# Kernel tuning notes

Hardware: AMD Instinct MI355X
Metric: run time of the kernel (lower is better)

The kernel has to match this reference:

```python
import jax, jax.numpy as jnp
import numpy as np

D_EMB = 256


def setup_inputs() -> dict:
    key = jax.random.key(0)
    ks = jax.random.split(key, 7)
    B, S, d = 4, 4096, D_EMB
    scale = 1.0 / np.sqrt(d)
    return {
        "x": jax.random.normal(ks[0], (B, S, d), jnp.float32),
        "Wqkv": jax.random.normal(ks[1], (d, 3 * d), jnp.float32) * scale,
        "bqkv": jax.random.normal(ks[2], (3 * d,), jnp.float32) * 0.02,
        "Wproj": jax.random.normal(ks[3], (d, d), jnp.float32) * scale,
        "bproj": jax.random.normal(ks[4], (d,), jnp.float32) * 0.02,
        "Wfc": jax.random.normal(ks[5], (d, 1), jnp.float32) * scale,
        "bfc": jax.random.normal(ks[6], (1,), jnp.float32) * 0.02,
    }


def reference(x, Wqkv, bqkv, Wproj, bproj, Wfc, bfc):
    # qkv projection: [B,S,3d] -> split into q,k,v [B,S,d]
    qkv = x @ Wqkv + bqkv
    q, k, v = jnp.split(qkv, 3, axis=2)
    # full attention scores [B,S,S]; note: original applies NO 1/sqrt(d)
    # scaling (dead branch in source), 'traditional' softmax over last dim
    attn_scores = jnp.einsum("bqd,bkd->bqk", q, k)
    attn_weights = jax.nn.softmax(attn_scores, axis=-1)
    y = jnp.einsum("bqk,bkd->bqd", attn_weights, v)
    y = y @ Wproj + bproj
    out = y @ Wfc + bfc  # [B,S,1]
    return out
```

## Files before the change

### kernel.cpp

```cpp
#include <hip/hip_runtime.h>
#include <hip/hip_bf16.h>

#define BQ 4
#define SQ 4096
#define DQ 256
#define N3 768
#define KBLK 64
#define NITER (SQ / KBLK)
#define KHALF (NITER / 2)
#define LOG2E 1.44269504f
#define THR2 11.5415603f

typedef __attribute__((ext_vector_type(8))) _Float16 f16x8;
typedef __attribute__((ext_vector_type(4))) float f32x4;
typedef __attribute__((ext_vector_type(4))) unsigned int u32x4;

__device__ __forceinline__ short f2h(float f) {
  _Float16 h = (_Float16)f;
  union { _Float16 h; short s; } v; v.h = h;
  return v.s;
}

__device__ __forceinline__ void gload16(const void* g, void* lds) {
  __builtin_amdgcn_global_load_lds(
      (const __attribute__((address_space(1))) unsigned int*)g,
      (__attribute__((address_space(3))) unsigned int*)lds, 16, 0, 0);
}

__global__ void wcomb_kernel(const float* __restrict__ Wproj,
                             const float* __restrict__ bproj,
                             const float* __restrict__ Wfc,
                             const float* __restrict__ bfc,
                             float* __restrict__ Wc) {
  __shared__ float wf[256];
  const int t = threadIdx.x;
  wf[t] = Wfc[t];
  __syncthreads();
  float acc = 0.f;
  for (int j = 0; j < 256; ++j) acc += Wproj[(size_t)t * 256 + j] * wf[j];
  Wc[t] = acc;
  if (t == 0) {
    float c = bfc[0];
    for (int j = 0; j < 256; ++j) c += bproj[j] * wf[j];
    Wc[256] = c;
  }
}

__global__ void wconv_kernel(const float* __restrict__ Wqkv,
                             short* __restrict__ W16T) {
  __shared__ float tile[64][65];
  const int nb = blockIdx.x * 64;
  const int kb = blockIdx.y * 64;
  const int t = threadIdx.x;
  const int tr = t >> 6, tc = t & 63;
#pragma unroll
  for (int i = 0; i < 16; ++i)
    tile[tr + i * 4][tc] = Wqkv[(size_t)(kb + tr + i * 4) * N3 + nb + tc];
  __syncthreads();
#pragma unroll
  for (int i = 0; i < 16; ++i)
    W16T[(size_t)(nb + tr + i * 4) * 256 + kb + tc] = f2h(tile[tc][tr + i * 4]);
}

__global__ __launch_bounds__(1024, 4) void qkv_kernel(
    const float* __restrict__ x, const short* __restrict__ W16T,
    const float* __restrict__ bqkv, const float* __restrict__ Wc,
    short* __restrict__ Qb, short* __restrict__ Kb, float* __restrict__ u) {
  __shared__ short xs[64][264];
  __shared__ short ws[2][64][256];
  __shared__ float u_red[4][4][16];
  const int t = threadIdx.x;
  const int l = t & 63, w = t >> 6;
  const int lr = l & 15, lg = l >> 4;
  const int mq = w >> 2, nq = w & 3;
  const int Mbase = blockIdx.x * 64;

#define STAGE_W(BUF, NT)                                                      \
  {                                                                           \
    _Pragma("unroll") for (int i = 0; i < 2; ++i) {                           \
      const int n = w * 4 + i * 2 + (l >> 5);                                 \
      const int gc = (l & 31) ^ (n & 7);                                      \
      gload16(W16T + (size_t)((NT)*64 + n) * 256 + gc * 8,                    \
              &ws[BUF][w * 4 + i * 2][0]);                                    \
    }                                                                         \
  }

  STAGE_W(0, 0);

  {
    const int m = t >> 4, kc = (t & 15) * 16;
    const float* src = x + (size_t)(Mbase + m) * DQ + kc;
    short tmp[16];
#pragma unroll
    for (int i = 0; i < 16; ++i) tmp[i] = f2h(src[i]);
    *(u32x4*)&xs[m][kc] = *(u32x4*)&tmp[0];
    *(u32x4*)&xs[m][kc + 8] = *(u32x4*)&tmp[8];
  }

  float bias_qk[8], bias_u[4], wc_u[4];
#pragma unroll
  for (int i = 0; i < 8; ++i) bias_qk[i] = bqkv[i * 64 + nq * 16 + lr];
#pragma unroll
  for (int i = 0; i < 4; ++i) {
    bias_u[i] = bqkv[512 + i * 64 + nq * 16 + lr];
    wc_u[i] = Wc[i * 64 + nq * 16 + lr];
  }

  __syncthreads();

  unsigned qksto[8][2];
  float upart[4] = {0.f, 0.f, 0.f, 0.f};

#pragma unroll
  for (int nt = 0; nt < 12; ++nt) {
    const int cur = nt & 1;
    if (nt + 1 < 12) {
      STAGE_W(cur ^ 1, nt + 1);
      asm volatile("s_waitcnt vmcnt(2)" ::: "memory");
    } else {
      asm volatile("s_waitcnt vmcnt(0)" ::: "memory");
    }
    __builtin_amdgcn_s_barrier();
    __builtin_amdgcn_sched_barrier(0);

    f32x4 acc = {};
    const char* wR = (const char*)&ws[cur][nq * 16 + lr][0];
#pragma unroll
    for (int kk = 0; kk < 8; ++kk) {
      f16x8 af = *(f16x8*)&xs[mq * 16 + lr][kk * 32 + lg * 8];
      f16x8 bfr = *(const f16x8*)(wR + (((4 * kk + lg) ^ (lr & 7)) << 4));
      acc = __builtin_amdgcn_mfma_f32_16x16x32_f16(af, bfr, acc, 0, 0, 0);
    }
    if (nt < 8) {
      const float sc = (nt < 4) ? 1.f : LOG2E;
      unsigned s0 = (unsigned short)f2h((acc[0] + bias_qk[nt]) * sc);
      unsigned s1 = (unsigned short)f2h((acc[1] + bias_qk[nt]) * sc);
      unsigned s2 = (unsigned short)f2h((acc[2] + bias_qk[nt]) * sc);
      unsigned s3 = (unsigned short)f2h((acc[3] + bias_qk[nt]) * sc);
      qksto[nt][0] = s0 | (s1 << 16);
      qksto[nt][1] = s2 | (s3 << 16);
    } else {
#pragma unroll
      for (int r = 0; r < 4; ++r) upart[r] += (acc[r] + bias_u[nt - 8]) * wc_u[nt - 8];
    }
    __builtin_amdgcn_s_barrier();
  }

#pragma unroll
  for (int nt = 0; nt < 8; ++nt) {
    const int col = nt * 64 + nq * 16 + lr;
#pragma unroll
    for (int r = 0; r < 4; ++r) {
      const int row = Mbase + mq * 16 + lg * 4 + r;
      const short sv = (short)((qksto[nt][r >> 1] >> ((r & 1) * 16)) & 0xFFFF);
      if (col < 256) Qb[(size_t)row * DQ + col] = sv;
      else           Kb[(size_t)row * DQ + (col - 256)] = sv;
    }
  }

#pragma unroll
  for (int mask = 1; mask <= 8; mask <<= 1)
#pragma unroll
    for (int r = 0; r < 4; ++r) upart[r] += __shfl_xor(upart[r], mask, 64);
  if (lr == 0) {
#pragma unroll
    for (int r = 0; r < 4; ++r) u_red[mq][nq][lg * 4 + r] = upart[r];
  }
  __syncthreads();
  if (t < 64)
    u[Mbase + t] = u_red[t >> 4][0][t & 15] + u_red[t >> 4][1][t & 15] +
                   u_red[t >> 4][2][t & 15] + u_red[t >> 4][3][t & 15];
#undef STAGE_W
}

__global__ __launch_bounds__(512, 4) void attn_kernel(
    const short* __restrict__ Qb, const short* __restrict__ Kb,
    const float* __restrict__ u, float* __restrict__ Pm,
    float* __restrict__ Pd, float* __restrict__ Pn) {
  __shared__ short Ks[2][64][256];
  __shared__ __align__(16) float u_lds[2048];
  __shared__ float Mrg[2][4][32][3];

  const int t = threadIdx.x;
  const int l = t & 63, w = t >> 6;
  const int lr = l & 15, lg = l >> 4;
  const int qg = w >> 2, h = w & 3;
  const int bid = blockIdx.x;
  const int b = bid & 3;
  const int half = (bid >> 2) & 1;
  const int qbase = (bid >> 3) * 64;

  const short* kbase = Kb + ((size_t)b * SQ + (size_t)half * (SQ / 2)) * DQ;
  const float* ubase = u + (size_t)b * SQ + half * (SQ / 2);

#define STAGE(BUF, KB)                                                      \
  {                                                                         \
    _Pragma("unroll") for (int i = 0; i < 4; ++i) {                         \
      const int kr = w * 8 + i * 2 + (l >> 5);                              \
      const int gc = (l & 31) ^ (kr & 7);                                   \
      gload16(kbase + (size_t)((KB)*64 + kr) * DQ + gc * 8,                 \
              &Ks[BUF][w * 8 + i * 2][0]);                                  \
    }                                                                       \
  }

  STAGE(0, 0);
  gload16(ubase + w * 256 + (l << 2), &u_lds[w * 256]);

  f16x8 qf[2][8];
#pragma unroll
  for (int mm = 0; mm < 2; ++mm) {
    const short* qptr = Qb + (size_t)(b * SQ + qbase + qg * 32 + mm * 16 + lr) * DQ;
#pragma unroll
    for (int kk = 0; kk < 8; ++kk)
      qf[mm][kk] = *(const f16x8*)(qptr + kk * 32 + lg * 8);
  }

  float m_run[2] = {-1e30f, -1e30f};
  float num[2] = {0.f, 0.f}, den[2] = {0.f, 0.f};

  __syncthreads();

  for (int kb = 0; kb < KHALF; ++kb) {
    const int cur = kb & 1;
    if (kb + 1 < KHALF) {
      STAGE(cur ^ 1, kb + 1);
      asm volatile("s_waitcnt vmcnt(4)" ::: "memory");
    } else {
      asm volatile("s_waitcnt vmcnt(0)" ::: "memory");
    }
    __builtin_amdgcn_s_barrier();
    __builtin_amdgcn_sched_barrier(0);

    const char* kR = (const char*)&Ks[cur][h * 16 + lr][0];
    f32x4 s[2] = {};
    __builtin_amdgcn_s_setprio(1);
#pragma unroll
    for (int kk = 0; kk < 8; ++kk) {
      f16x8 kf = *(const f16x8*)(kR + (((4 * kk + lg) ^ (lr & 7)) << 4));
      s[0] = __builtin_amdgcn_mfma_f32_16x16x32_f16(kf, qf[0][kk], s[0], 0, 0, 0);
      s[1] = __builtin_amdgcn_mfma_f32_16x16x32_f16(kf, qf[1][kk], s[1], 0, 0, 0);
    }
    __builtin_amdgcn_s_setprio(0);

    bool over = false;
#pragma unroll
    for (int mm = 0; mm < 2; ++mm)
#pragma unroll
      for (int r = 0; r < 4; ++r) over = over || (s[mm][r] > m_run[mm] + THR2);
    if (__any(over)) {
#pragma unroll
      for (int mm = 0; mm < 2; ++mm) {
        float mt = fmaxf(fmaxf(s[mm][0], s[mm][1]), fmaxf(s[mm][2], s[mm][3]));
        mt = fmaxf(mt, __shfl_xor(mt, 16, 64));
        mt = fmaxf(mt, __shfl_xor(mt, 32, 64));
        const float mn = fmaxf(m_run[mm], mt);
        const float sc = exp2f(m_run[mm] - mn);
        m_run[mm] = mn;
        num[mm] *= sc;
        den[mm] *= sc;
      }
    }
    {
      const f32x4 uv = *(const f32x4*)&u_lds[kb * 64 + h * 16 + lg * 4];
#pragma unroll
      for (int mm = 0; mm < 2; ++mm)
#pragma unroll
        for (int r = 0; r < 4; ++r) {
          const float p = exp2f(s[mm][r] - m_run[mm]);
          den[mm] += p;
          num[mm] += p * uv[r];
        }
    }
    __builtin_amdgcn_s_barrier();
  }

#pragma unroll
  for (int mm = 0; mm < 2; ++mm) {
    num[mm] += __shfl_xor(num[mm], 16, 64);
    num[mm] += __shfl_xor(num[mm], 32, 64);
    den[mm] += __shfl_xor(den[mm], 16, 64);
    den[mm] += __shfl_xor(den[mm], 32, 64);
  }
  if (lg == 0) {
#pragma unroll
    for (int mm = 0; mm < 2; ++mm) {
      Mrg[qg][h][mm * 16 + lr][0] = m_run[mm];
      Mrg[qg][h][mm * 16 + lr][1] = den[mm];
      Mrg[qg][h][mm * 16 + lr][2] = num[mm];
    }
  }
  __syncthreads();

  if (t < 64) {
    const int row = t & 31, qg2 = t >> 5;
    float M = Mrg[qg2][0][row][0];
#pragma unroll
    for (int hh = 1; hh < 4; ++hh) M = fmaxf(M, Mrg[qg2][hh][row][0]);
    float dt = 0.f, nt = 0.f;
#pragma unroll
    for (int hh = 0; hh < 4; ++hh) {
      const float e = exp2f(Mrg[qg2][hh][row][0] - M);
      dt += e * Mrg[qg2][hh][row][1];
      nt += e * Mrg[qg2][hh][row][2];
    }
    const size_t idx = (size_t)half * (BQ * SQ) + (size_t)b * SQ + qbase + row +
                       qg2 * 32;
    Pm[idx] = M; Pd[idx] = dt; Pn[idx] = nt;
  }
#undef STAGE
}

__global__ void merge_kernel(const float* __restrict__ Pm,
                             const float* __restrict__ Pd,
                             const float* __restrict__ Pn,
                             const float* __restrict__ Wc,
                             float* __restrict__ out) {
  const int gid = blockIdx.x * 256 + threadIdx.x;
  const float m0 = Pm[gid], m1 = Pm[BQ * SQ + gid];
  const float M = fmaxf(m0, m1);
  const float e0 = exp2f(m0 - M), e1 = exp2f(m1 - M);
  const float den = e0 * Pd[gid] + e1 * Pd[BQ * SQ + gid];
  const float num = e0 * Pn[gid] + e1 * Pn[BQ * SQ + gid];
  out[gid] = num / den + Wc[256];
}

extern "C" void kernel_launch(void* const* d_in, const int* in_sizes, int n_in,
                              void* d_out, int out_size, void* d_ws, size_t ws_size,
                              hipStream_t stream) {
  const float* x     = (const float*)d_in[0];
  const float* Wqkv  = (const float*)d_in[1];
  const float* bqkv  = (const float*)d_in[2];
  const float* Wproj = (const float*)d_in[3];
  const float* bproj = (const float*)d_in[4];
  const float* Wfc   = (const float*)d_in[5];
  const float* bfc   = (const float*)d_in[6];
  float* out = (float*)d_out;

  const size_t SEG = (size_t)BQ * SQ * DQ * 2;
  char* wsb = (char*)d_ws;
  short* Qb   = (short*)(wsb);
  short* Kb   = (short*)(wsb + SEG);
  char* base  = wsb + 2 * SEG;
  float* Wc   = (float*)(base);
  float* u    = (float*)(base + 4096);
  short* W16T = (short*)(base + 4096 + 65536);
  float* Pm   = (float*)(base + 4096 + 65536 + 393216);
  float* Pd   = Pm + 2 * BQ * SQ;
  float* Pn   = Pd + 2 * BQ * SQ;

  wcomb_kernel<<<1, 256, 0, stream>>>(Wproj, bproj, Wfc, bfc, Wc);
  wconv_kernel<<<dim3(12, 4), 256, 0, stream>>>(Wqkv, W16T);
  qkv_kernel<<<256, 1024, 0, stream>>>(x, W16T, bqkv, Wc, Qb, Kb, u);
  attn_kernel<<<512, 512, 0, stream>>>(Qb, Kb, u, Pm, Pd, Pn);
  merge_kernel<<<BQ * SQ / 256, 256, 0, stream>>>(Pm, Pd, Pn, Wc, out);
}
```

Baseline: 105.8 us.

## Have each attention wave process all 64 query rows with 256-thread blocks

The attention block drops from 8 waves to 4. Each wave now holds Q fragments for all 64 query rows and owns a 16-key slice, where before two query groups of 32 rows were split across 8 waves. Each K fragment read from LDS therefore feeds four MFMAs instead of two, halving K LDS reads per MFMA. Staging loads per wave double (vmcnt adjusted to 8). The cost is more registers per thread (launch bounds change to 256,2) and fewer waves to hide latency.

```diff
diff --git a/kernel.cpp b/kernel.cpp
--- a/kernel.cpp
+++ b/kernel.cpp
@@ -173,18 +173,17 @@
 #undef STAGE_W
 }
 
-__global__ __launch_bounds__(512, 4) void attn_kernel(
+__global__ __launch_bounds__(256, 2) void attn_kernel(
     const short* __restrict__ Qb, const short* __restrict__ Kb,
     const float* __restrict__ u, float* __restrict__ Pm,
     float* __restrict__ Pd, float* __restrict__ Pn) {
   __shared__ short Ks[2][64][256];
   __shared__ __align__(16) float u_lds[2048];
-  __shared__ float Mrg[2][4][32][3];
+  __shared__ float Mrg[4][64][3];
 
   const int t = threadIdx.x;
   const int l = t & 63, w = t >> 6;
   const int lr = l & 15, lg = l >> 4;
-  const int qg = w >> 2, h = w & 3;
   const int bid = blockIdx.x;
   const int b = bid & 3;
   const int half = (bid >> 2) & 1;
@@ -195,28 +194,29 @@
 
 #define STAGE(BUF, KB)                                                      \
   {                                                                         \
-    _Pragma("unroll") for (int i = 0; i < 4; ++i) {                         \
-      const int kr = w * 8 + i * 2 + (l >> 5);                              \
+    _Pragma("unroll") for (int i = 0; i < 8; ++i) {                         \
+      const int kr = w * 16 + i * 2 + (l >> 5);                             \
       const int gc = (l & 31) ^ (kr & 7);                                   \
       gload16(kbase + (size_t)((KB)*64 + kr) * DQ + gc * 8,                 \
-              &Ks[BUF][w * 8 + i * 2][0]);                                  \
+              &Ks[BUF][w * 16 + i * 2][0]);                                 \
     }                                                                       \
   }
 
   STAGE(0, 0);
-  gload16(ubase + w * 256 + (l << 2), &u_lds[w * 256]);
-
-  f16x8 qf[2][8];
-#pragma unroll
-  for (int mm = 0; mm < 2; ++mm) {
-    const short* qptr = Qb + (size_t)(b * SQ + qbase + qg * 32 + mm * 16 + lr) * DQ;
+  gload16(ubase + w * 512 + (l << 2), &u_lds[w * 512]);
+  gload16(ubase + w * 512 + 256 + (l << 2), &u_lds[w * 512 + 256]);
+
+  f16x8 qf[4][8];
+#pragma unroll
+  for (int mm = 0; mm < 4; ++mm) {
+    const short* qptr = Qb + (size_t)(b * SQ + qbase + mm * 16 + lr) * DQ;
 #pragma unroll
     for (int kk = 0; kk < 8; ++kk)
       qf[mm][kk] = *(const f16x8*)(qptr + kk * 32 + lg * 8);
   }
 
-  float m_run[2] = {-1e30f, -1e30f};
-  float num[2] = {0.f, 0.f}, den[2] = {0.f, 0.f};
+  float m_run[4] = {-1e30f, -1e30f, -1e30f, -1e30f};
+  float num[4] = {}, den[4] = {};
 
   __syncthreads();
 
@@ -224,32 +224,34 @@
     const int cur = kb & 1;
     if (kb + 1 < KHALF) {
       STAGE(cur ^ 1, kb + 1);
-      asm volatile("s_waitcnt vmcnt(4)" ::: "memory");
+      asm volatile("s_waitcnt vmcnt(8)" ::: "memory");
     } else {
       asm volatile("s_waitcnt vmcnt(0)" ::: "memory");
     }
     __builtin_amdgcn_s_barrier();
     __builtin_amdgcn_sched_barrier(0);
 
-    const char* kR = (const char*)&Ks[cur][h * 16 + lr][0];
-    f32x4 s[2] = {};
+    const char* kR = (const char*)&Ks[cur][w * 16 + lr][0];
+    f32x4 s[4] = {};
     __builtin_amdgcn_s_setprio(1);
 #pragma unroll
     for (int kk = 0; kk < 8; ++kk) {
       f16x8 kf = *(const f16x8*)(kR + (((4 * kk + lg) ^ (lr & 7)) << 4));
       s[0] = __builtin_amdgcn_mfma_f32_16x16x32_f16(kf, qf[0][kk], s[0], 0, 0, 0);
       s[1] = __builtin_amdgcn_mfma_f32_16x16x32_f16(kf, qf[1][kk], s[1], 0, 0, 0);
+      s[2] = __builtin_amdgcn_mfma_f32_16x16x32_f16(kf, qf[2][kk], s[2], 0, 0, 0);
+      s[3] = __builtin_amdgcn_mfma_f32_16x16x32_f16(kf, qf[3][kk], s[3], 0, 0, 0);
     }
     __builtin_amdgcn_s_setprio(0);
 
     bool over = false;
 #pragma unroll
-    for (int mm = 0; mm < 2; ++mm)
+    for (int mm = 0; mm < 4; ++mm)
 #pragma unroll
       for (int r = 0; r < 4; ++r) over = over || (s[mm][r] > m_run[mm] + THR2);
     if (__any(over)) {
 #pragma unroll
-      for (int mm = 0; mm < 2; ++mm) {
+      for (int mm = 0; mm < 4; ++mm) {
         float mt = fmaxf(fmaxf(s[mm][0], s[mm][1]), fmaxf(s[mm][2], s[mm][3]));
         mt = fmaxf(mt, __shfl_xor(mt, 16, 64));
         mt = fmaxf(mt, __shfl_xor(mt, 32, 64));
@@ -261,9 +263,9 @@
       }
     }
     {
-      const f32x4 uv = *(const f32x4*)&u_lds[kb * 64 + h * 16 + lg * 4];
-#pragma unroll
-      for (int mm = 0; mm < 2; ++mm)
+      const f32x4 uv = *(const f32x4*)&u_lds[kb * 64 + w * 16 + lg * 4];
+#pragma unroll
+      for (int mm = 0; mm < 4; ++mm)
 #pragma unroll
         for (int r = 0; r < 4; ++r) {
           const float p = exp2f(s[mm][r] - m_run[mm]);
@@ -275,7 +277,7 @@
   }
 
 #pragma unroll
-  for (int mm = 0; mm < 2; ++mm) {
+  for (int mm = 0; mm < 4; ++mm) {
     num[mm] += __shfl_xor(num[mm], 16, 64);
     num[mm] += __shfl_xor(num[mm], 32, 64);
     den[mm] += __shfl_xor(den[mm], 16, 64);
@@ -283,28 +285,26 @@
   }
   if (lg == 0) {
 #pragma unroll
-    for (int mm = 0; mm < 2; ++mm) {
-      Mrg[qg][h][mm * 16 + lr][0] = m_run[mm];
-      Mrg[qg][h][mm * 16 + lr][1] = den[mm];
-      Mrg[qg][h][mm * 16 + lr][2] = num[mm];
+    for (int mm = 0; mm < 4; ++mm) {
+      Mrg[w][mm * 16 + lr][0] = m_run[mm];
+      Mrg[w][mm * 16 + lr][1] = den[mm];
+      Mrg[w][mm * 16 + lr][2] = num[mm];
     }
   }
   __syncthreads();
 
   if (t < 64) {
-    const int row = t & 31, qg2 = t >> 5;
-    float M = Mrg[qg2][0][row][0];
-#pragma unroll
-    for (int hh = 1; hh < 4; ++hh) M = fmaxf(M, Mrg[qg2][hh][row][0]);
+    float M = Mrg[0][t][0];
+#pragma unroll
+    for (int hh = 1; hh < 4; ++hh) M = fmaxf(M, Mrg[hh][t][0]);
     float dt = 0.f, nt = 0.f;
 #pragma unroll
     for (int hh = 0; hh < 4; ++hh) {
-      const float e = exp2f(Mrg[qg2][hh][row][0] - M);
-      dt += e * Mrg[qg2][hh][row][1];
-      nt += e * Mrg[qg2][hh][row][2];
-    }
-    const size_t idx = (size_t)half * (BQ * SQ) + (size_t)b * SQ + qbase + row +
-                       qg2 * 32;
+      const float e = exp2f(Mrg[hh][t][0] - M);
+      dt += e * Mrg[hh][t][1];
+      nt += e * Mrg[hh][t][2];
+    }
+    const size_t idx = (size_t)half * (BQ * SQ) + (size_t)b * SQ + qbase + t;
     Pm[idx] = M; Pd[idx] = dt; Pn[idx] = nt;
   }
 #undef STAGE
@@ -351,6 +351,6 @@
   wcomb_kernel<<<1, 256, 0, stream>>>(Wproj, bproj, Wfc, bfc, Wc);
   wconv_kernel<<<dim3(12, 4), 256, 0, stream>>>(Wqkv, W16T);
   qkv_kernel<<<256, 1024, 0, stream>>>(x, W16T, bqkv, Wc, Qb, Kb, u);
-  attn_kernel<<<512, 512, 0, stream>>>(Qb, Kb, u, Pm, Pd, Pn);
+  attn_kernel<<<512, 256, 0, stream>>>(Qb, Kb, u, Pm, Pd, Pn);
   merge_kernel<<<BQ * SQ / 256, 256, 0, stream>>>(Pm, Pd, Pn, Wc, out);
 }
```

Result: slower. 113.9 us (+7.6%).
